# Performance work log

Measured on AMD Instinct MI355X. Metric: run time of the kernel, lower is better.

## Reference

```python
import jax, jax.numpy as jnp
import numpy as np

D_MODEL = 1024
D_STATE = 64
CHUNK = 256
BATCH = 4
SEQ_LEN = 4096


def setup_inputs() -> dict:
    key = jax.random.key(0)
    k1, k2, k3, k4, k5 = jax.random.split(key, 5)
    u = jax.random.normal(k1, (BATCH, SEQ_LEN, D_MODEL), jnp.float32)
    delta = jax.random.uniform(k2, (BATCH, SEQ_LEN, D_MODEL), jnp.float32)
    B = jax.random.normal(k3, (BATCH, SEQ_LEN, D_STATE), jnp.float32)
    C = jax.random.normal(k4, (BATCH, SEQ_LEN, D_STATE), jnp.float32)
    # matches nn.init.uniform_(A_log, -3.0, -1.0)
    A_log = jax.random.uniform(k5, (D_STATE, D_MODEL), jnp.float32, minval=-3.0, maxval=-1.0)
    return {"u": u, "delta": delta, "B": B, "C": C, "A_log": A_log}


def reference(u, delta, B, C, A_log):
    # delta is accepted but unused, as in the original forward.
    batch, seq_len, d_model = u.shape
    d_state = A_log.shape[0]
    n_chunks = seq_len // CHUNK  # seq_len chosen divisible by chunk_size
    A = -jnp.exp(A_log)  # (N, D)

    # Split sequence into chunks; hidden state resets at each chunk boundary,
    # so all chunks scan independently (vectorized over the n_chunks axis).
    # time-major layout for lax.scan: (CHUNK, batch, n_chunks, ...)
    uc = jnp.moveaxis(u.reshape(batch, n_chunks, CHUNK, d_model), 2, 0)
    Bc = jnp.moveaxis(B.reshape(batch, n_chunks, CHUNK, d_state), 2, 0)
    Cc = jnp.moveaxis(C.reshape(batch, n_chunks, CHUNK, d_state), 2, 0)

    h0 = jnp.zeros((batch, n_chunks, d_state, d_model), u.dtype)

    def step(h, inp):
        x_t, B_t, C_t = inp  # (b,c,D), (b,c,N), (b,c,N)
        h = A * h + B_t[..., :, None] * x_t[..., None, :]  # (b,c,N,D)
        y = jnp.einsum('bcn,bcnd->bcd', C_t, h)             # (b,c,D)
        return h, y

    _, ys = jax.lax.scan(step, h0, (uc, Bc, Cc))  # (CHUNK, b, n_chunks, D)
    out = jnp.moveaxis(ys, 0, 2).reshape(batch, seq_len, d_model)
    return out
```

## Files before the change

### kernel.cpp

```cpp
#include <hip/hip_runtime.h>

typedef float v4 __attribute__((ext_vector_type(4)));

#define D_MODEL 1024
#define D_STATE 64
#define CHUNK   256
#define TILE_T  64

__global__ __launch_bounds__(256, 1)
void YvParallelScan_kernel(const float* __restrict__ u,
                           const float* __restrict__ B,
                           const float* __restrict__ C,
                           const float* __restrict__ A_log,
                           float* __restrict__ out) {
    __shared__ v4 sB[TILE_T * 16];
    __shared__ v4 sC[TILE_T * 16];
    __shared__ v4 sP[2][4][64];

    const int bc   = blockIdx.x >> 2;
    const int dq   = blockIdx.x & 3;
    const int tid  = threadIdx.x;
    const int ng   = tid >> 6;
    const int lane = tid & 63;
    const int rowbase = bc * CHUNK;

    const v4* Bg = (const v4*)(B + (size_t)rowbase * D_STATE);
    const v4* Cg = (const v4*)(C + (size_t)rowbase * D_STATE);

    const int dbase4 = dq * 64 + lane;

    v4 a4[16], h4[16];
#pragma unroll
    for (int j = 0; j < 16; ++j) {
        const int n = ng * 16 + j;
        v4 al = ((const v4*)A_log)[n * 256 + dbase4];
        v4 na;
        na[0] = -__expf(al[0]); na[1] = -__expf(al[1]);
        na[2] = -__expf(al[2]); na[3] = -__expf(al[3]);
        a4[j] = na;
        v4 z = {0.f, 0.f, 0.f, 0.f};
        h4[j] = z;
    }

    const v4* uptr = (const v4*)(u + (size_t)rowbase * D_MODEL) + dbase4;
    v4*       optr = (v4*)(out + (size_t)rowbase * D_MODEL) + dbase4;

    v4 xa = uptr[0];
    v4 xb = uptr[256];

    for (int ti = 0; ti < CHUNK / TILE_T; ++ti) {
#pragma unroll
        for (int k = 0; k < 4; ++k) {
            sB[k * 256 + tid] = Bg[ti * 1024 + k * 256 + tid];
            sC[k * 256 + tid] = Cg[ti * 1024 + k * 256 + tid];
        }
        __syncthreads();

#pragma unroll 4
        for (int tl = 0; tl < TILE_T; ++tl) {
            const int t  = ti * TILE_T + tl;
            const int tp = (t + 2 < CHUNK) ? (t + 2) : (CHUNK - 1);
            v4 xn = uptr[(size_t)tp * 256];

            const v4 x = xa;
            v4 acc = {0.f, 0.f, 0.f, 0.f};
#pragma unroll
            for (int jj = 0; jj < 4; ++jj) {
                v4 b4 = sB[tl * 16 + ng * 4 + jj];
                v4 c4 = sC[tl * 16 + ng * 4 + jj];
#pragma unroll
                for (int k = 0; k < 4; ++k) {
                    const int j = jj * 4 + k;
                    h4[j] = a4[j] * h4[j] + b4[k] * x;
                    acc  += c4[k] * h4[j];
                }
            }

            const int slot = t & 1;
            const int red  = t & 3;
            if (ng != red) sP[slot][ng][lane] = acc;
            __syncthreads();
            if (ng == red) {
                v4 s = acc;
#pragma unroll
                for (int w = 0; w < 4; ++w)
                    if (w != red) s += sP[slot][w][lane];
                optr[(size_t)t * 256] = s;
            }
            xa = xb; xb = xn;
        }
    }
}

extern "C" void kernel_launch(void* const* d_in, const int* in_sizes, int n_in,
                              void* d_out, int out_size, void* d_ws, size_t ws_size,
                              hipStream_t stream) {
    const float* u     = (const float*)d_in[0];
    const float* B     = (const float*)d_in[2];
    const float* C     = (const float*)d_in[3];
    const float* A_log = (const float*)d_in[4];
    float* out = (float*)d_out;

    YvParallelScan_kernel<<<256, 256, 0, stream>>>(u, B, C, A_log, out);
}
```

Before: 268.0 us.

## Remap threads to scalar d with 4-lane state split and shuffle reduction

Each block now covers 64 d-columns, and a group of 4 adjacent lanes splits the 64 state entries, with the per-step output reduced by warp shuffles instead of shared memory plus a per-timestep __syncthreads. The grid grows from 256 to 1024 blocks and launch bounds allow 4 blocks per CU, which should improve occupancy and remove the barrier stalls on every timestep. In exchange, global loads of u and A_log become scalar and only partly coalesced: each group of 4 lanes reads the same address, so a wavefront touches 16 distinct floats. The new __syncthreads at the end of each tile also guards the shared B/C buffers before they are reloaded.

```diff
diff --git a/kernel.cpp b/kernel.cpp
--- a/kernel.cpp
+++ b/kernel.cpp
@@ -7,7 +7,7 @@
 #define CHUNK   256
 #define TILE_T  64
 
-__global__ __launch_bounds__(256, 1)
+__global__ __launch_bounds__(256, 4)
 void YvParallelScan_kernel(const float* __restrict__ u,
                            const float* __restrict__ B,
                            const float* __restrict__ C,
@@ -15,38 +15,32 @@
                            float* __restrict__ out) {
     __shared__ v4 sB[TILE_T * 16];
     __shared__ v4 sC[TILE_T * 16];
-    __shared__ v4 sP[2][4][64];
 
-    const int bc   = blockIdx.x >> 2;
-    const int dq   = blockIdx.x & 3;
-    const int tid  = threadIdx.x;
-    const int ng   = tid >> 6;
-    const int lane = tid & 63;
+    const int bid = blockIdx.x;
+    const int bc  = bid >> 4;
+    const int ds  = bid & 15;
+    const int tid = threadIdx.x;
+    const int ng  = tid & 3;
+    const int dq  = tid >> 2;
+    const int d   = ds * 64 + dq;
     const int rowbase = bc * CHUNK;
 
     const v4* Bg = (const v4*)(B + (size_t)rowbase * D_STATE);
     const v4* Cg = (const v4*)(C + (size_t)rowbase * D_STATE);
 
-    const int dbase4 = dq * 64 + lane;
-
-    v4 a4[16], h4[16];
+    float a[16], h[16];
 #pragma unroll
     for (int j = 0; j < 16; ++j) {
         const int n = ng * 16 + j;
-        v4 al = ((const v4*)A_log)[n * 256 + dbase4];
-        v4 na;
-        na[0] = -__expf(al[0]); na[1] = -__expf(al[1]);
-        na[2] = -__expf(al[2]); na[3] = -__expf(al[3]);
-        a4[j] = na;
-        v4 z = {0.f, 0.f, 0.f, 0.f};
-        h4[j] = z;
+        a[j] = -__expf(A_log[n * D_MODEL + d]);
+        h[j] = 0.f;
     }
 
-    const v4* uptr = (const v4*)(u + (size_t)rowbase * D_MODEL) + dbase4;
-    v4*       optr = (v4*)(out + (size_t)rowbase * D_MODEL) + dbase4;
+    const float* uptr = u + (size_t)rowbase * D_MODEL + d;
+    float*       optr = out + (size_t)rowbase * D_MODEL + d;
 
-    v4 xa = uptr[0];
-    v4 xb = uptr[256];
+    float xa = uptr[0];
+    float xb = uptr[D_MODEL];
 
     for (int ti = 0; ti < CHUNK / TILE_T; ++ti) {
 #pragma unroll
@@ -60,35 +54,29 @@
         for (int tl = 0; tl < TILE_T; ++tl) {
             const int t  = ti * TILE_T + tl;
             const int tp = (t + 2 < CHUNK) ? (t + 2) : (CHUNK - 1);
-            v4 xn = uptr[(size_t)tp * 256];
+            const float xn = uptr[(size_t)tp * D_MODEL];
 
-            const v4 x = xa;
-            v4 acc = {0.f, 0.f, 0.f, 0.f};
+            const float x = xa;
+            float acc0 = 0.f, acc1 = 0.f;
 #pragma unroll
             for (int jj = 0; jj < 4; ++jj) {
-                v4 b4 = sB[tl * 16 + ng * 4 + jj];
-                v4 c4 = sC[tl * 16 + ng * 4 + jj];
+                const v4 b4 = sB[tl * 16 + ng * 4 + jj];
+                const v4 c4 = sC[tl * 16 + ng * 4 + jj];
 #pragma unroll
                 for (int k = 0; k < 4; ++k) {
                     const int j = jj * 4 + k;
-                    h4[j] = a4[j] * h4[j] + b4[k] * x;
-                    acc  += c4[k] * h4[j];
+                    h[j] = a[j] * h[j] + b4[k] * x;
+                    if (k & 1) acc1 += c4[k] * h[j];
+                    else       acc0 += c4[k] * h[j];
                 }
             }
-
-            const int slot = t & 1;
-            const int red  = t & 3;
-            if (ng != red) sP[slot][ng][lane] = acc;
-            __syncthreads();
-            if (ng == red) {
-                v4 s = acc;
-#pragma unroll
-                for (int w = 0; w < 4; ++w)
-                    if (w != red) s += sP[slot][w][lane];
-                optr[(size_t)t * 256] = s;
-            }
+            float acc = acc0 + acc1;
+            acc += __shfl_xor(acc, 1);
+            acc += __shfl_xor(acc, 2);
+            if (ng == 0) optr[(size_t)t * D_MODEL] = acc;
             xa = xb; xb = xn;
         }
+        __syncthreads();
     }
 }
 
@@ -101,5 +89,5 @@
     const float* A_log = (const float*)d_in[4];
     float* out = (float*)d_out;
 
-    YvParallelScan_kernel<<<256, 256, 0, stream>>>(u, B, C, A_log, out);
+    YvParallelScan_kernel<<<1024, 256, 0, stream>>>(u, B, C, A_log, out);
 }
```

Result: faster. 259.6 us (-3.2%).
